# Performance work log

Measured on AMD Instinct MI355X. Metric: run time of the kernel, lower is better.

## Reference

```python
import jax, jax.numpy as jnp
import numpy as np

QDEPTH = 8
WIDTH = 64
HEIGHT = 64
WIRES = 12  # ceil(log2(64*64))
BATCH = 1024


def setup_inputs() -> dict:
    key = jax.random.key(0)
    k1, k2 = jax.random.split(key)
    x = jax.random.normal(k1, (BATCH, 1, WIDTH, HEIGHT), dtype=jnp.float32)
    # torch.nn.Parameter(torch.randn(weight_shape) * 0.4)
    weights = jax.random.normal(k2, (QDEPTH, WIRES, 3), dtype=jnp.float32) * 0.4
    return {"x": x, "weights": weights, "reps": 1}


def _rot_matrices(angles):
    # angles: (L, W, 3) -> (L, W, 2, 2) complex64; Rot(phi, theta, omega) = RZ(omega) RY(theta) RZ(phi)
    phi, theta, omega = angles[..., 0], angles[..., 1], angles[..., 2]
    c = jnp.cos(theta * 0.5).astype(jnp.complex64)
    s = jnp.sin(theta * 0.5).astype(jnp.complex64)
    ep = jnp.exp(-0.5j * (phi + omega).astype(jnp.complex64))  # e^{-i(phi+omega)/2}
    em = jnp.exp(-0.5j * (phi - omega).astype(jnp.complex64))  # e^{-i(phi-omega)/2}
    row0 = jnp.stack([ep * c, -jnp.conj(em) * s], axis=-1)
    row1 = jnp.stack([em * s, jnp.conj(ep) * c], axis=-1)
    return jnp.stack([row0, row1], axis=-2)


def _apply_1q(state, U, wire):
    # state: (B, 2, 2, ..., 2); apply 2x2 U on axis wire+1
    ax = wire + 1
    s = jnp.moveaxis(state, ax, -1)
    s = s @ U.T  # out[..., i] = sum_j U[i, j] s[..., j]
    return jnp.moveaxis(s, -1, ax)


def _apply_cnot(state, control, target):
    c, t = control + 1, target + 1
    s0, s1 = jnp.split(state, 2, axis=c)   # control = 0 / 1 halves
    s1 = jnp.flip(s1, axis=t)              # X on target where control = 1
    return jnp.concatenate([s0, s1], axis=c)


def _sel_layer(state, mats_l, r):
    # one StronglyEntanglingLayers layer: Rot on every wire, then CNOT ring of range r
    for w in range(WIRES):
        state = _apply_1q(state, mats_l[w], w)
    for w in range(WIRES):
        state = _apply_cnot(state, w, (w + r) % WIRES)
    return state


def _circuit(state, weights, reps):
    mats = _rot_matrices(jnp.tanh(weights))  # qw_map.tanh applied to raw weights
    for _ in range(reps):
        for l in range(QDEPTH):
            r = (l % (WIRES - 1)) + 1  # PennyLane default ranges
            layer = jax.checkpoint(lambda s, m, _r=r: _sel_layer(s, m, _r))
            state = layer(state, mats[l])
    return state


def reference(x, weights, reps):
    b = x.shape[0]
    v = x.reshape(b, -1)  # (b, 4096)
    norm = jnp.linalg.norm(v, axis=-1, keepdims=True)
    v = (v / norm).astype(jnp.complex64)
    state = v.reshape((b,) + (2,) * WIRES)
    state = _circuit(state, weights, reps)
    out = state.reshape(b, -1) * norm
    return out.reshape(b, 1, WIDTH, HEIGHT)
```

## Files before the change

### kernel.cpp

```cpp
#include <hip/hip_runtime.h>

#define WIRES   12
#define NSTATE  4096
#define QDEPTH  8
#define BLOCK   64
#define PER_T   64

using f2 = __attribute__((ext_vector_type(2))) float;

__device__ __forceinline__ int pad(int i) { return i + (i >> 6); }

constexpr int colF(int l, int j) {
    int rr = (l % (WIRES - 1)) + 1;
    int v = 1 << j;
    for (int k = WIRES - 1; k >= 0; --k) {
        int bc = 11 - k;
        int bt = 11 - ((k + rr) % WIRES);
        v ^= ((v >> bc) & 1) << bt;
    }
    return v;
}
struct ColsT { int v[QDEPTH][WIRES]; };
constexpr ColsT mkCols() {
    ColsT c{};
    for (int l = 0; l < QDEPTH; ++l)
        for (int j = 0; j < WIRES; ++j) c.v[l][j] = colF(l, j);
    return c;
}
static __device__ const ColsT COLS = mkCols();

template<int P>
__device__ __forceinline__ void gate(f2 r[PER_T], const float* __restrict__ m)
{
    const float4 A = ((const float4*)m)[0];
    const float4 B = ((const float4*)m)[1];
    #pragma unroll
    for (int pr = 0; pr < PER_T / 2; ++pr) {
        const int k0 = ((pr >> P) << (P + 1)) | (pr & ((1 << P) - 1));
        const int k1 = k0 | (1 << P);
        const f2 s0 = r[k0], s1 = r[k1];
        const f2 p0 = f2{-s0.y, s0.x};
        const f2 p1 = f2{-s1.y, s1.x};
        r[k0] = A.x * s0 + A.y * p0 + A.z * s1 + A.w * p1;
        r[k1] = B.x * s0 + B.y * p0 + B.z * s1 + B.w * p1;
    }
}

__global__ __launch_bounds__(BLOCK, 2) void qsim_kernel(
    const float* __restrict__ x,
    const float* __restrict__ wts,
    const int*   __restrict__ reps_ptr,
    float*       __restrict__ out,
    int write_mode)
{
    __shared__ f2 st[65 * 64];
    __shared__ __align__(16) float mats[QDEPTH * WIRES][8];

    const int lane = threadIdx.x;
    const int b    = blockIdx.x;

    for (int t = lane; t < QDEPTH * WIRES; t += BLOCK) {
        float phi   = tanhf(wts[t * 3 + 0]);
        float theta = tanhf(wts[t * 3 + 1]);
        float omega = tanhf(wts[t * 3 + 2]);
        float c  = cosf(theta * 0.5f);
        float s  = sinf(theta * 0.5f);
        float a  = 0.5f * (phi + omega);
        float bm = 0.5f * (phi - omega);
        float ca = cosf(a),  sa = sinf(a);
        float cb = cosf(bm), sb = sinf(bm);
        mats[t][0] =  c * ca;
        mats[t][1] = -c * sa;
        mats[t][2] = -s * cb;
        mats[t][3] = -s * sb;
        mats[t][4] =  s * cb;
        mats[t][5] = -s * sb;
        mats[t][6] =  c * ca;
        mats[t][7] =  c * sa;
    }

    const float4* xb4 = (const float4*)(x + (size_t)b * NSTATE);
    #pragma unroll
    for (int c = 0; c < 16; ++c) {
        int g = c * BLOCK + lane;
        float4 v = xb4[g];
        st[pad(2 * g)]     = f2{v.x, v.y};
        st[pad(2 * g + 1)] = f2{v.z, v.w};
    }
    f2 r[PER_T];
    #pragma unroll
    for (int m = 0; m < 32; ++m) {
        f2 pr2 = st[pad((lane << 5) | m)];
        r[2*m]   = f2{pr2.x, 0.f};
        r[2*m+1] = f2{pr2.y, 0.f};
    }

    const int reps = reps_ptr[0];
    for (int rep = 0; rep < reps; ++rep) {
        #pragma unroll 1
        for (int l = 0; l < QDEPTH; ++l) {
            const float* M = &mats[l * WIRES][0];

            gate<5>(r, M + 6*8);  gate<4>(r, M + 7*8);
            gate<3>(r, M + 8*8);  gate<2>(r, M + 9*8);
            gate<1>(r, M + 10*8); gate<0>(r, M + 11*8);

            #pragma unroll
            for (int k = 0; k < PER_T; ++k) st[65 * lane + k] = r[k];
            #pragma unroll
            for (int k = 0; k < PER_T; ++k) r[k] = st[65 * k + lane];

            gate<5>(r, M + 0*8); gate<4>(r, M + 1*8);
            gate<3>(r, M + 2*8); gate<2>(r, M + 3*8);
            gate<1>(r, M + 4*8); gate<0>(r, M + 5*8);

            #pragma unroll
            for (int k = 0; k < PER_T; ++k) st[65 * k + lane] = r[k];

            const int c0 = COLS.v[l][0], c1 = COLS.v[l][1], c2 = COLS.v[l][2];
            const int c3 = COLS.v[l][3], c4 = COLS.v[l][4], c5 = COLS.v[l][5];
            int Ft = 0;
            #pragma unroll
            for (int j = 0; j < 6; ++j)
                Ft ^= ((lane >> j) & 1) ? COLS.v[l][6 + j] : 0;
            #pragma unroll
            for (int k = 0; k < PER_T; ++k) {
                int ck = ((k & 1)  ? c0 : 0) ^ ((k & 2)  ? c1 : 0) ^
                         ((k & 4)  ? c2 : 0) ^ ((k & 8)  ? c3 : 0) ^
                         ((k & 16) ? c4 : 0) ^ ((k & 32) ? c5 : 0);
                r[k] = st[pad(Ft ^ ck)];
            }
        }
    }

    if (write_mode == 0) {
        #pragma unroll
        for (int m = 0; m < 32; ++m)
            st[pad((lane << 5) | m)] = f2{r[2*m].x, r[2*m+1].x};
        float4* ob4 = (float4*)(out + (size_t)b * NSTATE);
        #pragma unroll
        for (int c = 0; c < 16; ++c) {
            int g = c * BLOCK + lane;
            f2 a  = st[pad(2 * g)];
            f2 b2 = st[pad(2 * g + 1)];
            ob4[g] = make_float4(a.x, a.y, b2.x, b2.y);
        }
    } else {
        float2* ob = (float2*)out + (size_t)b * NSTATE;
        #pragma unroll
        for (int k = 0; k < PER_T; ++k)
            ob[(lane << 6) | k] = make_float2(r[k].x, r[k].y);
    }
}

extern "C" void kernel_launch(void* const* d_in, const int* in_sizes, int n_in,
                              void* d_out, int out_size, void* d_ws, size_t ws_size,
                              hipStream_t stream) {
    const float* x    = (const float*)d_in[0];
    const float* wts  = (const float*)d_in[1];
    const int*   reps = (const int*)d_in[2];
    float*       out  = (float*)d_out;
    (void)in_sizes; (void)n_in; (void)d_ws; (void)ws_size;

    const int write_mode = (out_size >= 2 * 1024 * NSTATE) ? 1 : 0;

    qsim_kernel<<<1024, BLOCK, 0, stream>>>(x, wts, reps, out, write_mode);
}
```

Before: 167.1 us.

## Precompute gate matrices in a separate kernel and use packed-FMA inline asm

Moves the tanh/sin/cos gate-matrix construction into a small prologue kernel that writes pre-arranged packed coefficient pairs to workspace, so each block no longer recomputes them. The 2x2 complex gate is rewritten as hand-scheduled v_pk_mul/v_pk_fma inline assembly over two pairs at a time, using op_sel to swap real and imaginary parts instead of building rotated copies. Launch bounds are relaxed to one block per SM, which allows more registers but may lower occupancy. Matrices are now read from global memory rather than LDS, and an extra kernel launch is added.

```diff
diff --git a/kernel.cpp b/kernel.cpp
--- a/kernel.cpp
+++ b/kernel.cpp
@@ -29,55 +29,78 @@
 }
 static __device__ const ColsT COLS = mkCols();
 
+__global__ void mats_kernel(const float* __restrict__ wts, f2* __restrict__ mg)
+{
+    int t = blockIdx.x * blockDim.x + threadIdx.x;
+    if (t >= QDEPTH * WIRES) return;
+    float phi   = tanhf(wts[t * 3 + 0]);
+    float theta = tanhf(wts[t * 3 + 1]);
+    float omega = tanhf(wts[t * 3 + 2]);
+    float c  = cosf(theta * 0.5f);
+    float s  = sinf(theta * 0.5f);
+    float a  = 0.5f * (phi + omega);
+    float bm = 0.5f * (phi - omega);
+    float ca = cosf(a),  sa = sinf(a);
+    float cb = cosf(bm), sb = sinf(bm);
+    f2* m = mg + t * 8;
+    m[0] = f2{ c * ca,  c * ca};
+    m[1] = f2{ c * sa, -c * sa};
+    m[2] = f2{-s * cb, -s * cb};
+    m[3] = f2{ s * sb, -s * sb};
+    m[4] = f2{ s * cb,  s * cb};
+    m[5] = f2{ s * sb, -s * sb};
+    m[6] = f2{ c * ca,  c * ca};
+    m[7] = f2{-c * sa,  c * sa};
+}
+
 template<int P>
-__device__ __forceinline__ void gate(f2 r[PER_T], const float* __restrict__ m)
+__device__ __forceinline__ void gate(f2 r[PER_T], const f2* __restrict__ m)
 {
-    const float4 A = ((const float4*)m)[0];
-    const float4 B = ((const float4*)m)[1];
+    const f2 u00r = m[0], u00w = m[1], u01r = m[2], u01w = m[3];
+    const f2 u10r = m[4], u10w = m[5], u11r = m[6], u11w = m[7];
     #pragma unroll
-    for (int pr = 0; pr < PER_T / 2; ++pr) {
+    for (int pr = 0; pr < PER_T / 2; pr += 2) {
         const int k0 = ((pr >> P) << (P + 1)) | (pr & ((1 << P) - 1));
         const int k1 = k0 | (1 << P);
-        const f2 s0 = r[k0], s1 = r[k1];
-        const f2 p0 = f2{-s0.y, s0.x};
-        const f2 p1 = f2{-s1.y, s1.x};
-        r[k0] = A.x * s0 + A.y * p0 + A.z * s1 + A.w * p1;
-        r[k1] = B.x * s0 + B.y * p0 + B.z * s1 + B.w * p1;
+        const int q  = pr + 1;
+        const int j0 = ((q >> P) << (P + 1)) | (q & ((1 << P) - 1));
+        const int j1 = j0 | (1 << P);
+        f2 a0, b0, a1, b1;
+        asm("v_pk_mul_f32 %0, %4, %8\n\t"
+            "v_pk_mul_f32 %1, %4, %12\n\t"
+            "v_pk_mul_f32 %2, %6, %8\n\t"
+            "v_pk_mul_f32 %3, %6, %12\n\t"
+            "v_pk_fma_f32 %0, %4, %9, %0 op_sel:[1,0,0] op_sel_hi:[0,1,1]\n\t"
+            "v_pk_fma_f32 %1, %4, %13, %1 op_sel:[1,0,0] op_sel_hi:[0,1,1]\n\t"
+            "v_pk_fma_f32 %2, %6, %9, %2 op_sel:[1,0,0] op_sel_hi:[0,1,1]\n\t"
+            "v_pk_fma_f32 %3, %6, %13, %3 op_sel:[1,0,0] op_sel_hi:[0,1,1]\n\t"
+            "v_pk_fma_f32 %0, %5, %10, %0\n\t"
+            "v_pk_fma_f32 %1, %5, %14, %1\n\t"
+            "v_pk_fma_f32 %2, %7, %10, %2\n\t"
+            "v_pk_fma_f32 %3, %7, %14, %3\n\t"
+            "v_pk_fma_f32 %0, %5, %11, %0 op_sel:[1,0,0] op_sel_hi:[0,1,1]\n\t"
+            "v_pk_fma_f32 %1, %5, %15, %1 op_sel:[1,0,0] op_sel_hi:[0,1,1]\n\t"
+            "v_pk_fma_f32 %2, %7, %11, %2 op_sel:[1,0,0] op_sel_hi:[0,1,1]\n\t"
+            "v_pk_fma_f32 %3, %7, %15, %3 op_sel:[1,0,0] op_sel_hi:[0,1,1]"
+            : "=&v"(a0), "=&v"(b0), "=&v"(a1), "=&v"(b1)
+            : "v"(r[k0]), "v"(r[k1]), "v"(r[j0]), "v"(r[j1]),
+              "v"(u00r), "v"(u00w), "v"(u01r), "v"(u01w),
+              "v"(u10r), "v"(u10w), "v"(u11r), "v"(u11w));
+        r[k0] = a0; r[k1] = b0; r[j0] = a1; r[j1] = b1;
     }
 }
 
-__global__ __launch_bounds__(BLOCK, 2) void qsim_kernel(
+__global__ __launch_bounds__(BLOCK, 1) void qsim_kernel(
     const float* __restrict__ x,
-    const float* __restrict__ wts,
+    const f2*    __restrict__ mats_g,
     const int*   __restrict__ reps_ptr,
     float*       __restrict__ out,
     int write_mode)
 {
     __shared__ f2 st[65 * 64];
-    __shared__ __align__(16) float mats[QDEPTH * WIRES][8];
 
     const int lane = threadIdx.x;
     const int b    = blockIdx.x;
-
-    for (int t = lane; t < QDEPTH * WIRES; t += BLOCK) {
-        float phi   = tanhf(wts[t * 3 + 0]);
-        float theta = tanhf(wts[t * 3 + 1]);
-        float omega = tanhf(wts[t * 3 + 2]);
-        float c  = cosf(theta * 0.5f);
-        float s  = sinf(theta * 0.5f);
-        float a  = 0.5f * (phi + omega);
-        float bm = 0.5f * (phi - omega);
-        float ca = cosf(a),  sa = sinf(a);
-        float cb = cosf(bm), sb = sinf(bm);
-        mats[t][0] =  c * ca;
-        mats[t][1] = -c * sa;
-        mats[t][2] = -s * cb;
-        mats[t][3] = -s * sb;
-        mats[t][4] =  s * cb;
-        mats[t][5] = -s * sb;
-        mats[t][6] =  c * ca;
-        mats[t][7] =  c * sa;
-    }
 
     const float4* xb4 = (const float4*)(x + (size_t)b * NSTATE);
     #pragma unroll
@@ -99,7 +122,7 @@
     for (int rep = 0; rep < reps; ++rep) {
         #pragma unroll 1
         for (int l = 0; l < QDEPTH; ++l) {
-            const float* M = &mats[l * WIRES][0];
+            const f2* M = mats_g + l * WIRES * 8;
 
             gate<5>(r, M + 6*8);  gate<4>(r, M + 7*8);
             gate<3>(r, M + 8*8);  gate<2>(r, M + 9*8);
@@ -160,9 +183,11 @@
     const float* wts  = (const float*)d_in[1];
     const int*   reps = (const int*)d_in[2];
     float*       out  = (float*)d_out;
-    (void)in_sizes; (void)n_in; (void)d_ws; (void)ws_size;
+    f2*          mg   = (f2*)d_ws;
+    (void)in_sizes; (void)n_in; (void)ws_size;
 
     const int write_mode = (out_size >= 2 * 1024 * NSTATE) ? 1 : 0;
 
-    qsim_kernel<<<1024, BLOCK, 0, stream>>>(x, wts, reps, out, write_mode);
+    mats_kernel<<<1, 128, 0, stream>>>(wts, mg);
+    qsim_kernel<<<1024, BLOCK, 0, stream>>>(x, mg, reps, out, write_mode);
 }
```

New measurement: 154.8 us. -7.3%, faster.
